# Kernel tuning notes

Measured on AMD Instinct MI355X. Metric: run time of the kernel, lower is better.

Reference implementation:

```python
import jax, jax.numpy as jnp
import numpy as np

N_GENES = 15135
K = int(np.ceil(0.5 * N_GENES))  # 7568, PyG TopKPooling ratio=0.5
BS, E, F_IN, H, HF, NC, L = 8, 242160, 64, 128, 512, 2, 3


def setup_inputs() -> dict:
    key = jax.random.key(0)
    ks = jax.random.split(key, 16)
    def lin(k, fin, fout):
        s = 1.0 / np.sqrt(fin)
        return jax.random.normal(k, (fin, fout), jnp.float32) * s
    x = jax.random.normal(ks[0], (BS, N_GENES, F_IN), jnp.float32)
    batch = jnp.zeros((BS,), jnp.int32)
    edge_index = jax.random.randint(ks[1], (2, E), 0, N_GENES, dtype=jnp.int32)
    CAT = L * H
    return {
        "x": x,
        "batch": batch,
        "edge_index": edge_index,
        "W1": lin(ks[2], F_IN, H), "b1": jnp.zeros((H,), jnp.float32),
        "W2": lin(ks[3], H, H),    "b2": jnp.zeros((H,), jnp.float32),
        "W3": lin(ks[4], H, H),    "b3": jnp.zeros((H,), jnp.float32),
        "topk_w": jax.random.normal(ks[5], (CAT,), jnp.float32) / np.sqrt(CAT),
        "fcW": lin(ks[6], CAT, 1), "fcb": jnp.zeros((1,), jnp.float32),
        "lin1W": lin(ks[7], K, HF), "lin1b": jnp.zeros((HF,), jnp.float32),
        "lin2W": lin(ks[8], HF, NC), "lin2b": jnp.zeros((NC,), jnp.float32),
    }


def reference(x, batch, edge_index, W1, b1, W2, b2, W3, b3,
              topk_w, fcW, fcb, lin1W, lin1b, lin2W, lin2b):
    bs = x.shape[0]
    # --- GCN normalization with self-loops (PyG GCNConv defaults) ---
    loop = jnp.arange(N_GENES, dtype=edge_index.dtype)
    src = jnp.concatenate([edge_index[0], loop])
    dst = jnp.concatenate([edge_index[1], loop])
    deg = jnp.zeros((N_GENES,), x.dtype).at[dst].add(1.0)
    dinv = jax.lax.rsqrt(deg)  # deg >= 1 due to self-loops
    norm = dinv[src] * dinv[dst]  # [E+N]

    def gcn(h, W, b):
        h = h @ W                                   # [bs, N, H]
        msg = h[:, src, :] * norm[None, :, None]    # gather + edge weight
        agg = jnp.zeros_like(h).at[:, dst, :].add(msg)  # scatter-add
        return agg + b

    h1 = jax.nn.relu(gcn(x, W1, b1))
    h2 = jax.nn.relu(gcn(h1, W2, b2))
    h3 = jax.nn.relu(gcn(h2, W3, b3))
    # mode='cat': stack on last dim then flatten -> feature order (H, layer)
    xc = jnp.stack([h1, h2, h3], -1).reshape(bs, N_GENES, -1)  # [bs, N, L*H]

    # --- TopKPooling (score = tanh(x.w/||w||), keep top ceil(0.5*N)) ---
    score = jnp.tanh((xc @ topk_w) / jnp.linalg.norm(topk_w))  # [bs, N]
    top_s, perm = jax.lax.top_k(score, K)                       # [bs, K]
    xp = jnp.take_along_axis(xc, perm[..., None], axis=1) * top_s[..., None]

    z = (xp @ fcW + fcb)[..., 0]          # [bs, K]
    h = jax.nn.relu(z @ lin1W + lin1b)    # [bs, HF]; dropout inactive (eval)
    logits = h @ lin2W + lin2b            # [bs, NC]
    return jax.nn.log_softmax(logits, axis=-1)
```

## Files before the change

### kernel.cpp

```cpp
#include <hip/hip_runtime.h>

#define N_G   15135
#define E_N   242160
#define BSZ   8
#define K_TOP 7568
#define NH    128
#define NBIN  65536
#define SUFS  65600

typedef float f4v __attribute__((ext_vector_type(4)));

__global__ void zero_kernel(int* __restrict__ p, int n) {
  int i = blockIdx.x * 1024 + threadIdx.x;
  if (i < n) p[i] = 0;
}

__global__ void count_kernel(const int* __restrict__ ei, int* __restrict__ cnt) {
  int e = blockIdx.x * 256 + threadIdx.x;
  if (e < E_N) atomicAdd(&cnt[ei[E_N + e]], 1);
}

__global__ __launch_bounds__(1024) void scan_kernel(const int* __restrict__ cnt,
                                                    int* __restrict__ rowstart,
                                                    float* __restrict__ dinv,
                                                    int* __restrict__ gctr,
                                                    const float* __restrict__ topk_w,
                                                    float* __restrict__ scal) {
  __shared__ int buf[1024];
  __shared__ int base;
  int tid = threadIdx.x;
  int i = blockIdx.x * 1024 + tid;
  int v = (i < N_G) ? cnt[i] : 0;
  if (i < N_G) dinv[i] = 1.0f / sqrtf((float)(v + 1));
  buf[tid] = v;
  __syncthreads();
  for (int s = 1; s < 1024; s <<= 1) {
    int t = (tid >= s) ? buf[tid - s] : 0;
    __syncthreads();
    buf[tid] += t;
    __syncthreads();
  }
  if (tid == 1023) base = atomicAdd(gctr, buf[1023]);
  __syncthreads();
  if (i < N_G) rowstart[i] = base + buf[tid] - v;
  if (blockIdx.x == 0) {
    __shared__ float fbuf[512];
    if (tid < 512) {
      float w = (tid < 384) ? topk_w[tid] : 0.f;
      fbuf[tid] = w * w;
    }
    __syncthreads();
    for (int s = 256; s > 0; s >>= 1) {
      if (tid < s) fbuf[tid] += fbuf[tid + s];
      __syncthreads();
    }
    if (tid == 0) scal[0] = 1.0f / sqrtf(fbuf[0]);
  }
}

__global__ void fill_kernel(const int* __restrict__ ei, const int* __restrict__ rowstart,
                            int* __restrict__ fillc, int* __restrict__ csr) {
  int e = blockIdx.x * 256 + threadIdx.x;
  if (e < E_N) {
    int s = ei[e], d = ei[E_N + e];
    int pos = rowstart[d] + atomicAdd(&fillc[d], 1);
    csr[pos] = s;
  }
}

template<int CIN, bool BR>
__global__ __launch_bounds__(256, 6) void mm_kernel(const float* __restrict__ A,
                                                    const float* __restrict__ W,
                                                    const float* __restrict__ bias,
                                                    float* __restrict__ out) {
  __shared__ float Bst[32][132];
  __shared__ float Ast2[32][68];
  int tid = threadIdx.x;
  int b = blockIdx.x & 7;
  int ib = blockIdx.x >> 3;
  int rb0 = b * N_G + ib * 64;
  int rmax = N_G - ib * 64;
  int c0 = (tid & 31) * 4;
  int r0 = (tid >> 5) * 8;
  float acc[8][4];
#pragma unroll
  for (int i = 0; i < 8; i++)
#pragma unroll
    for (int j = 0; j < 4; j++) acc[i][j] = 0.f;

  for (int k0 = 0; k0 < CIN; k0 += 32) {
    {
      int koff = (tid & 7) * 4;
      int row = tid >> 3;
#pragma unroll
      for (int p = 0; p < 2; ++p) {
        int r = row + p * 32;
        f4v v = {0.f, 0.f, 0.f, 0.f};
        if (r < rmax) v = __builtin_nontemporal_load((const f4v*)(A + (size_t)(rb0 + r) * CIN + k0 + koff));
        Ast2[koff + 0][r] = v.x; Ast2[koff + 1][r] = v.y;
        Ast2[koff + 2][r] = v.z; Ast2[koff + 3][r] = v.w;
      }
    }
    {
      int cc = (tid & 31) * 4;
      int kr = tid >> 5;
#pragma unroll
      for (int p = 0; p < 4; ++p) {
        int k = kr + p * 8;
        *(float4*)&Bst[k][cc] = *(const float4*)(W + (size_t)(k0 + k) * NH + cc);
      }
    }
    __syncthreads();
#pragma unroll 4
    for (int kk = 0; kk < 32; ++kk) {
      float a[8], bb[4];
      *(float4*)&a[0] = *(const float4*)&Ast2[kk][r0];
      *(float4*)&a[4] = *(const float4*)&Ast2[kk][r0 + 4];
      *(float4*)&bb[0] = *(const float4*)&Bst[kk][c0];
#pragma unroll
      for (int i = 0; i < 8; i++)
#pragma unroll
        for (int j = 0; j < 4; j++)
          acc[i][j] = fmaf(a[i], bb[j], acc[i][j]);
    }
    __syncthreads();
  }
  float b0 = 0.f, b1 = 0.f, b2 = 0.f, b3 = 0.f;
  if (BR) { b0 = bias[c0]; b1 = bias[c0+1]; b2 = bias[c0+2]; b3 = bias[c0+3]; }
#pragma unroll
  for (int i = 0; i < 8; i++) {
    int r = r0 + i;
    if (r < rmax) {
      float4 v;
      if (BR) {
        v.x = fmaxf(acc[i][0] + b0, 0.f); v.y = fmaxf(acc[i][1] + b1, 0.f);
        v.z = fmaxf(acc[i][2] + b2, 0.f); v.w = fmaxf(acc[i][3] + b3, 0.f);
      } else {
        v.x = acc[i][0]; v.y = acc[i][1]; v.z = acc[i][2]; v.w = acc[i][3];
      }
      *(float4*)(out + (size_t)(rb0 + r) * NH + c0) = v;
    }
  }
}

template<int CH, bool BR>
__global__ __launch_bounds__(256) void agg_h_kernel(const float* __restrict__ src,
                                                    const int* __restrict__ csr,
                                                    const int* __restrict__ rowstart,
                                                    const int* __restrict__ cnt,
                                                    const float* __restrict__ dinv,
                                                    const float* __restrict__ bias,
                                                    float* __restrict__ dst, int half) {
  int b = blockIdx.x & 7;
  int chunk = blockIdx.x >> 3;
  int wave = threadIdx.x >> 6, lane = threadIdx.x & 63;
  int d = chunk * 4 + wave;
  if (d >= N_G) return;
  d = __builtin_amdgcn_readfirstlane(d);
  int c = (CH == 128) ? ((half << 6) + lane) : lane;
  const float* sb = src + (size_t)b * N_G * CH;
  float dv = dinv[d];
  int e0 = rowstart[d];
  int n = cnt[d];
  const int* ce = csr + e0;
  float acc[8];
  acc[0] = dv * sb[(size_t)d * CH + c];
#pragma unroll
  for (int k = 1; k < 8; ++k) acc[k] = 0.f;
  int l = 0;
  for (; l + 16 <= n; l += 16) {
    int ss[16]; float ww[16], vv[16];
#pragma unroll
    for (int k = 0; k < 16; ++k) ss[k] = ce[l + k];
#pragma unroll
    for (int k = 0; k < 16; ++k) ww[k] = dinv[ss[k]];
#pragma unroll
    for (int k = 0; k < 16; ++k) vv[k] = sb[(size_t)ss[k] * CH + c];
#pragma unroll
    for (int k = 0; k < 16; ++k) acc[k & 7] = fmaf(ww[k], vv[k], acc[k & 7]);
  }
  for (; l + 8 <= n; l += 8) {
    int ss[8]; float ww[8], vv[8];
#pragma unroll
    for (int k = 0; k < 8; ++k) ss[k] = ce[l + k];
#pragma unroll
    for (int k = 0; k < 8; ++k) ww[k] = dinv[ss[k]];
#pragma unroll
    for (int k = 0; k < 8; ++k) vv[k] = sb[(size_t)ss[k] * CH + c];
#pragma unroll
    for (int k = 0; k < 8; ++k) acc[k] = fmaf(ww[k], vv[k], acc[k]);
  }
  for (; l < n; ++l) {
    int s = ce[l];
    acc[0] = fmaf(dinv[s], sb[(size_t)s * CH + c], acc[0]);
  }
  float s = ((acc[0] + acc[1]) + (acc[2] + acc[3])) + ((acc[4] + acc[5]) + (acc[6] + acc[7]));
  float r = BR ? fmaxf(fmaf(dv, s, bias[c]), 0.f) : dv * s;
  __builtin_nontemporal_store(r, &dst[((size_t)b * N_G + d) * CH + c]);
}

__global__ __launch_bounds__(256) void agg_score_h_kernel(const float* __restrict__ hw,
                                                          const int* __restrict__ csr,
                                                          const int* __restrict__ rowstart,
                                                          const int* __restrict__ cnt,
                                                          const float* __restrict__ dinv,
                                                          const float* __restrict__ bias,
                                                          const float* __restrict__ h1,
                                                          const float* __restrict__ h2,
                                                          const float* __restrict__ topk_w,
                                                          const float* __restrict__ fcW,
                                                          float* __restrict__ pd1,
                                                          float* __restrict__ pd2, int half) {
  int b = blockIdx.x & 7;
  int chunk = blockIdx.x >> 3;
  int wave = threadIdx.x >> 6, lane = threadIdx.x & 63;
  int d = chunk * 4 + wave;
  if (d >= N_G) return;
  d = __builtin_amdgcn_readfirstlane(d);
  int c = (half << 6) + lane;
  const float* sb = hw + (size_t)b * N_G * NH;
  float dv = dinv[d];
  int e0 = rowstart[d];
  int n = cnt[d];
  const int* ce = csr + e0;
  float acc[8];
  acc[0] = dv * sb[(size_t)d * NH + c];
#pragma unroll
  for (int k = 1; k < 8; ++k) acc[k] = 0.f;
  int l = 0;
  for (; l + 16 <= n; l += 16) {
    int ss[16]; float ww[16], vv[16];
#pragma unroll
    for (int k = 0; k < 16; ++k) ss[k] = ce[l + k];
#pragma unroll
    for (int k = 0; k < 16; ++k) ww[k] = dinv[ss[k]];
#pragma unroll
    for (int k = 0; k < 16; ++k) vv[k] = sb[(size_t)ss[k] * NH + c];
#pragma unroll
    for (int k = 0; k < 16; ++k) acc[k & 7] = fmaf(ww[k], vv[k], acc[k & 7]);
  }
  for (; l + 8 <= n; l += 8) {
    int ss[8]; float ww[8], vv[8];
#pragma unroll
    for (int k = 0; k < 8; ++k) ss[k] = ce[l + k];
#pragma unroll
    for (int k = 0; k < 8; ++k) ww[k] = dinv[ss[k]];
#pragma unroll
    for (int k = 0; k < 8; ++k) vv[k] = sb[(size_t)ss[k] * NH + c];
#pragma unroll
    for (int k = 0; k < 8; ++k) acc[k] = fmaf(ww[k], vv[k], acc[k]);
  }
  for (; l < n; ++l) {
    int s = ce[l];
    acc[0] = fmaf(dinv[s], sb[(size_t)s * NH + c], acc[0]);
  }
  float s = ((acc[0] + acc[1]) + (acc[2] + acc[3])) + ((acc[4] + acc[5]) + (acc[6] + acc[7]));
  float r = fmaxf(fmaf(dv, s, bias[c]), 0.f);
  size_t rbase = ((size_t)b * N_G + d) * NH + c;
  float u1 = __builtin_nontemporal_load(h1 + rbase);
  float u2 = __builtin_nontemporal_load(h2 + rbase);
  float d1 = u1 * topk_w[c * 3] + u2 * topk_w[c * 3 + 1] + r * topk_w[c * 3 + 2];
  float d2 = u1 * fcW[c * 3]    + u2 * fcW[c * 3 + 1]    + r * fcW[c * 3 + 2];
#pragma unroll
  for (int sh = 32; sh > 0; sh >>= 1) {
    d1 += __shfl_down(d1, sh);
    d2 += __shfl_down(d2, sh);
  }
  if (lane == 0) {
    int gw = b * N_G + d;
    pd1[gw * 2 + half] = d1;
    pd2[gw * 2 + half] = d2;
  }
}

__global__ void combine_kernel(const float* __restrict__ pd1, const float* __restrict__ pd2,
                               const float* __restrict__ scal, float* __restrict__ score,
                               float* __restrict__ d2a, unsigned* __restrict__ keys,
                               int* __restrict__ hist) {
  int b = blockIdx.y;
  int i = blockIdx.x * 256 + threadIdx.x;
  if (i >= N_G) return;
  int gw = b * N_G + i;
  float d1 = pd1[2 * gw] + pd1[2 * gw + 1];
  float d2 = pd2[2 * gw] + pd2[2 * gw + 1];
  float sc = tanhf(d1 * scal[0]);
  score[gw] = sc;
  d2a[gw] = d2;
  unsigned u = __float_as_uint(sc);
  unsigned k32 = (u & 0x80000000u) ? ~u : (u | 0x80000000u);
  keys[gw] = k32;
  atomicAdd(&hist[b * NBIN + (int)(k32 >> 16)], 1);
}

__global__ __launch_bounds__(1024) void suffix_kernel(const int* __restrict__ hist,
                                                      int* __restrict__ suf) {
  __shared__ int buf[1024];
  int b = blockIdx.x;
  const int* hb = hist + b * NBIN;
  int* sb = suf + b * SUFS;
  int t = threadIdx.x;
  int base = t * 64;
  int s = 0;
  for (int k = 0; k < 64; ++k) s += hb[base + k];
  buf[t] = s;
  __syncthreads();
  for (int off = 1; off < 1024; off <<= 1) {
    int v = (t + off < 1024) ? buf[t + off] : 0;
    __syncthreads();
    buf[t] += v;
    __syncthreads();
  }
  int acc = buf[t] - s;
  if (t == 0) sb[NBIN] = 0;
  for (int k = 63; k >= 0; --k) {
    acc += hb[base + k];
    sb[base + k] = acc;
  }
}

__global__ void scatter_kernel(const unsigned* __restrict__ keys, int* __restrict__ hist,
                               const int* __restrict__ suf, int2* __restrict__ bucket) {
  int b = blockIdx.y;
  int i = blockIdx.x * 256 + threadIdx.x;
  if (i >= N_G) return;
  unsigned k = keys[b * N_G + i];
  int bin = (int)(k >> 16);
  int old = atomicSub(&hist[b * NBIN + bin], 1);
  int pos = suf[b * SUFS + bin + 1] + old - 1;
  bucket[b * N_G + pos] = make_int2((int)k, i);
}

__global__ void rank_z_kernel(const unsigned* __restrict__ keys, const int* __restrict__ suf,
                              const int2* __restrict__ bucket, const float* __restrict__ score,
                              const float* __restrict__ d2a, const float* __restrict__ fcb,
                              float* __restrict__ z) {
  int b = blockIdx.y;
  int i = blockIdx.x * 256 + threadIdx.x;
  if (i >= N_G) return;
  int gw = b * N_G + i;
  unsigned k = keys[gw];
  int bin = (int)(k >> 16);
  int lo = suf[b * SUFS + bin + 1];
  int hi = suf[b * SUFS + bin];
  int r = lo;
  const int2* bk = bucket + b * N_G;
  for (int p = lo; p < hi; ++p) {
    int2 e = bk[p];
    unsigned kj = (unsigned)e.x;
    r += (kj > k || (kj == k && e.y < i)) ? 1 : 0;
  }
  if (r < K_TOP) z[b * K_TOP + r] = fmaf(score[gw], d2a[gw], fcb[0]);
}

__global__ __launch_bounds__(256) void lin1_kernel(const float* __restrict__ z,
                                                   const float* __restrict__ W,
                                                   float* __restrict__ hpre) {
  __shared__ float zb[237];
  int b = blockIdx.y, rs = blockIdx.x;
  int r0 = rs * 237;
  int rn = K_TOP - r0; if (rn > 237) rn = 237;
  for (int q = threadIdx.x; q < rn; q += 256) zb[q] = z[b * K_TOP + r0 + q];
  __syncthreads();
  int c = threadIdx.x;
  float a0 = 0.f, a1 = 0.f;
  for (int r = 0; r < rn; ++r) {
    float zz = zb[r];
    const float* wr = W + (size_t)(r0 + r) * 512;
    a0 = fmaf(zz, wr[c], a0);
    a1 = fmaf(zz, wr[c + 256], a1);
  }
  atomicAdd(&hpre[b * 512 + c], a0);
  atomicAdd(&hpre[b * 512 + c + 256], a1);
}

__global__ __launch_bounds__(128) void lin2_kernel(const float* __restrict__ hpre,
                                                   const float* __restrict__ l1b,
                                                   const float* __restrict__ W2,
                                                   const float* __restrict__ l2b,
                                                   float* __restrict__ out) {
  int b = blockIdx.x, tid = threadIdx.x;
  float a0 = 0.f, a1 = 0.f;
  for (int j = tid; j < 512; j += 128) {
    float t = fmaxf(hpre[b * 512 + j] + l1b[j], 0.f);
    a0 = fmaf(t, W2[j * 2 + 0], a0);
    a1 = fmaf(t, W2[j * 2 + 1], a1);
  }
#pragma unroll
  for (int s = 32; s > 0; s >>= 1) {
    a0 += __shfl_down(a0, s);
    a1 += __shfl_down(a1, s);
  }
  __shared__ float red[2][2];
  if ((tid & 63) == 0) { red[tid >> 6][0] = a0; red[tid >> 6][1] = a1; }
  __syncthreads();
  if (tid == 0) {
    float l0 = red[0][0] + red[1][0] + l2b[0];
    float l1 = red[0][1] + red[1][1] + l2b[1];
    float m = fmaxf(l0, l1);
    float lse = m + logf(expf(l0 - m) + expf(l1 - m));
    out[b * 2 + 0] = l0 - lse;
    out[b * 2 + 1] = l1 - lse;
  }
}

extern "C" void kernel_launch(void* const* d_in, const int* in_sizes, int n_in,
                              void* d_out, int out_size, void* d_ws, size_t ws_size,
                              hipStream_t stream) {
  const float* x   = (const float*)d_in[0];
  const int*   ei  = (const int*)d_in[2];
  const float* W1  = (const float*)d_in[3];
  const float* b1  = (const float*)d_in[4];
  const float* W2  = (const float*)d_in[5];
  const float* b2  = (const float*)d_in[6];
  const float* W3  = (const float*)d_in[7];
  const float* b3  = (const float*)d_in[8];
  const float* tkw = (const float*)d_in[9];
  const float* fcW = (const float*)d_in[10];
  const float* fcb = (const float*)d_in[11];
  const float* l1W = (const float*)d_in[12];
  const float* l1b = (const float*)d_in[13];
  const float* l2W = (const float*)d_in[14];
  const float* l2b = (const float*)d_in[15];
  float* out = (float*)d_out;

  char* ws = (char*)d_ws;
  size_t off = 0;
  auto alloc = [&](size_t bytes) {
    char* p = ws + off;
    off += (bytes + 255) & ~(size_t)255;
    return p;
  };
  int*   cnt   = (int*)alloc(15136 * 4);
  int*   fillc = (int*)alloc(15136 * 4);
  int*   gctr  = (int*)alloc(256);
  float* hpre  = (float*)alloc(4096 * 4);
  int*   hist  = (int*)alloc((size_t)BSZ * NBIN * 4);
  int*   rowstart = (int*)alloc(15136 * 4);
  float* dinv  = (float*)alloc(15136 * 4);
  float* scal  = (float*)alloc(64);
  float* z     = (float*)alloc((size_t)BSZ * K_TOP * 4);
  float* score = (float*)alloc(121088 * 4);
  float* d2a   = (float*)alloc(121088 * 4);
  unsigned* keys = (unsigned*)alloc(121088 * 4);
  int*   suf   = (int*)alloc((size_t)BSZ * SUFS * 4);
  int2*  bucket = (int2*)alloc(121088 * 8);
  float* pd1   = (float*)alloc(121088 * 2 * 4);
  float* pd2   = (float*)alloc(121088 * 2 * 4);
  int*   csr   = (int*)alloc((size_t)E_N * 4);
  float* ax = (float*)alloc((size_t)BSZ * N_G * 64 * 4);
  float* hw = (float*)alloc((size_t)BSZ * N_G * NH * 4);
  float* h1 = (float*)alloc((size_t)BSZ * N_G * NH * 4);
  float* h2 = (float*)alloc((size_t)BSZ * N_G * NH * 4);
  (void)ws_size; (void)in_sizes; (void)n_in; (void)out_size;

  int zero_n = (int)(((char*)rowstart - (char*)cnt) / 4);
  zero_kernel<<<(zero_n + 1023) / 1024, 1024, 0, stream>>>(cnt, zero_n);
  count_kernel<<<(E_N + 255) / 256, 256, 0, stream>>>(ei, cnt);
  scan_kernel<<<(N_G + 1023) / 1024, 1024, 0, stream>>>(cnt, rowstart, dinv, gctr, tkw, scal);
  fill_kernel<<<(E_N + 255) / 256, 256, 0, stream>>>(ei, rowstart, fillc, csr);

  dim3 mmg(8 * 237);
  int aggblocks = 8 * ((N_G + 3) / 4);

  agg_h_kernel<64, false><<<aggblocks, 256, 0, stream>>>(x, csr, rowstart, cnt, dinv, nullptr, ax, 0);
  mm_kernel<64, true><<<mmg, 256, 0, stream>>>(ax, W1, b1, h1);
  mm_kernel<128, false><<<mmg, 256, 0, stream>>>(h1, W2, nullptr, hw);
  agg_h_kernel<128, true><<<aggblocks, 256, 0, stream>>>(hw, csr, rowstart, cnt, dinv, b2, h2, 0);
  agg_h_kernel<128, true><<<aggblocks, 256, 0, stream>>>(hw, csr, rowstart, cnt, dinv, b2, h2, 1);
  mm_kernel<128, false><<<mmg, 256, 0, stream>>>(h2, W3, nullptr, hw);
  agg_score_h_kernel<<<aggblocks, 256, 0, stream>>>(hw, csr, rowstart, cnt, dinv, b3,
                                                    h1, h2, tkw, fcW, pd1, pd2, 0);
  agg_score_h_kernel<<<aggblocks, 256, 0, stream>>>(hw, csr, rowstart, cnt, dinv, b3,
                                                    h1, h2, tkw, fcW, pd1, pd2, 1);

  dim3 ng((N_G + 255) / 256, BSZ);
  combine_kernel<<<ng, 256, 0, stream>>>(pd1, pd2, scal, score, d2a, keys, hist);
  suffix_kernel<<<BSZ, 1024, 0, stream>>>(hist, suf);
  scatter_kernel<<<ng, 256, 0, stream>>>(keys, hist, suf, bucket);
  rank_z_kernel<<<ng, 256, 0, stream>>>(keys, suf, bucket, score, d2a, fcb, z);

  dim3 l1g(32, BSZ);
  lin1_kernel<<<l1g, 256, 0, stream>>>(z, l1W, hpre);
  lin2_kernel<<<BSZ, 128, 0, stream>>>(hpre, l1b, l2W, l2b, out);
}
```

Measured before the change: 724.9 us.

## Pack edge weights into CSR, add row descriptors, software-pipeline gather loop

The CSR entries now store each source index together with its dinv weight as an int2. A packed int4 row descriptor (start, count, dinv) is also built, so the aggregation kernels no longer do a dependent dinv[src] gather or three separate row-metadata loads. The neighbor loop is rewritten as an 8-wide software pipeline that loads the next batch of indices and features while the current batch is being accumulated. The trade-offs are double the CSR storage and higher register pressure from the pipelined buffers.

```diff
diff --git a/kernel.cpp b/kernel.cpp
--- a/kernel.cpp
+++ b/kernel.cpp
@@ -23,6 +23,7 @@
 __global__ __launch_bounds__(1024) void scan_kernel(const int* __restrict__ cnt,
                                                     int* __restrict__ rowstart,
                                                     float* __restrict__ dinv,
+                                                    int4* __restrict__ rowdesc,
                                                     int* __restrict__ gctr,
                                                     const float* __restrict__ topk_w,
                                                     float* __restrict__ scal) {
@@ -31,7 +32,8 @@
   int tid = threadIdx.x;
   int i = blockIdx.x * 1024 + tid;
   int v = (i < N_G) ? cnt[i] : 0;
-  if (i < N_G) dinv[i] = 1.0f / sqrtf((float)(v + 1));
+  float di = 1.0f / sqrtf((float)(v + 1));
+  if (i < N_G) dinv[i] = di;
   buf[tid] = v;
   __syncthreads();
   for (int s = 1; s < 1024; s <<= 1) {
@@ -42,7 +44,11 @@
   }
   if (tid == 1023) base = atomicAdd(gctr, buf[1023]);
   __syncthreads();
-  if (i < N_G) rowstart[i] = base + buf[tid] - v;
+  if (i < N_G) {
+    int rs = base + buf[tid] - v;
+    rowstart[i] = rs;
+    rowdesc[i] = make_int4(rs, v, __float_as_int(di), 0);
+  }
   if (blockIdx.x == 0) {
     __shared__ float fbuf[512];
     if (tid < 512) {
@@ -59,12 +65,13 @@
 }
 
 __global__ void fill_kernel(const int* __restrict__ ei, const int* __restrict__ rowstart,
-                            int* __restrict__ fillc, int* __restrict__ csr) {
+                            const float* __restrict__ dinv, int* __restrict__ fillc,
+                            int2* __restrict__ csr) {
   int e = blockIdx.x * 256 + threadIdx.x;
   if (e < E_N) {
     int s = ei[e], d = ei[E_N + e];
     int pos = rowstart[d] + atomicAdd(&fillc[d], 1);
-    csr[pos] = s;
+    csr[pos] = make_int2(s, __float_as_int(dinv[s]));
   }
 }
 
@@ -145,10 +152,8 @@
 
 template<int CH, bool BR>
 __global__ __launch_bounds__(256) void agg_h_kernel(const float* __restrict__ src,
-                                                    const int* __restrict__ csr,
-                                                    const int* __restrict__ rowstart,
-                                                    const int* __restrict__ cnt,
-                                                    const float* __restrict__ dinv,
+                                                    const int2* __restrict__ csr,
+                                                    const int4* __restrict__ rowdesc,
                                                     const float* __restrict__ bias,
                                                     float* __restrict__ dst, int half) {
   int b = blockIdx.x & 7;
@@ -157,42 +162,41 @@
   int d = chunk * 4 + wave;
   if (d >= N_G) return;
   d = __builtin_amdgcn_readfirstlane(d);
+  int4 rd = rowdesc[d];
+  int e0 = rd.x, n = rd.y;
+  float dv = __int_as_float(rd.z);
   int c = (CH == 128) ? ((half << 6) + lane) : lane;
   const float* sb = src + (size_t)b * N_G * CH;
-  float dv = dinv[d];
-  int e0 = rowstart[d];
-  int n = cnt[d];
-  const int* ce = csr + e0;
+  const int2* ce = csr + e0;
   float acc[8];
   acc[0] = dv * sb[(size_t)d * CH + c];
 #pragma unroll
   for (int k = 1; k < 8; ++k) acc[k] = 0.f;
   int l = 0;
-  for (; l + 16 <= n; l += 16) {
-    int ss[16]; float ww[16], vv[16];
-#pragma unroll
-    for (int k = 0; k < 16; ++k) ss[k] = ce[l + k];
-#pragma unroll
-    for (int k = 0; k < 16; ++k) ww[k] = dinv[ss[k]];
-#pragma unroll
-    for (int k = 0; k < 16; ++k) vv[k] = sb[(size_t)ss[k] * CH + c];
-#pragma unroll
-    for (int k = 0; k < 16; ++k) acc[k & 7] = fmaf(ww[k], vv[k], acc[k & 7]);
-  }
-  for (; l + 8 <= n; l += 8) {
-    int ss[8]; float ww[8], vv[8];
-#pragma unroll
-    for (int k = 0; k < 8; ++k) ss[k] = ce[l + k];
-#pragma unroll
-    for (int k = 0; k < 8; ++k) ww[k] = dinv[ss[k]];
-#pragma unroll
-    for (int k = 0; k < 8; ++k) vv[k] = sb[(size_t)ss[k] * CH + c];
-#pragma unroll
-    for (int k = 0; k < 8; ++k) acc[k] = fmaf(ww[k], vv[k], acc[k]);
+  if (n >= 8) {
+    int2 pA[8]; float vA[8];
+#pragma unroll
+    for (int k = 0; k < 8; ++k) pA[k] = ce[k];
+#pragma unroll
+    for (int k = 0; k < 8; ++k) vA[k] = sb[(size_t)pA[k].x * CH + c];
+    l = 8;
+    for (; l + 8 <= n; l += 8) {
+      int2 pB[8]; float vB[8];
+#pragma unroll
+      for (int k = 0; k < 8; ++k) pB[k] = ce[l + k];
+#pragma unroll
+      for (int k = 0; k < 8; ++k) vB[k] = sb[(size_t)pB[k].x * CH + c];
+#pragma unroll
+      for (int k = 0; k < 8; ++k) acc[k] = fmaf(__int_as_float(pA[k].y), vA[k], acc[k]);
+#pragma unroll
+      for (int k = 0; k < 8; ++k) { pA[k] = pB[k]; vA[k] = vB[k]; }
+    }
+#pragma unroll
+    for (int k = 0; k < 8; ++k) acc[k] = fmaf(__int_as_float(pA[k].y), vA[k], acc[k]);
   }
   for (; l < n; ++l) {
-    int s = ce[l];
-    acc[0] = fmaf(dinv[s], sb[(size_t)s * CH + c], acc[0]);
+    int2 p = ce[l];
+    acc[0] = fmaf(__int_as_float(p.y), sb[(size_t)p.x * CH + c], acc[0]);
   }
   float s = ((acc[0] + acc[1]) + (acc[2] + acc[3])) + ((acc[4] + acc[5]) + (acc[6] + acc[7]));
   float r = BR ? fmaxf(fmaf(dv, s, bias[c]), 0.f) : dv * s;
@@ -200,10 +204,8 @@
 }
 
 __global__ __launch_bounds__(256) void agg_score_h_kernel(const float* __restrict__ hw,
-                                                          const int* __restrict__ csr,
-                                                          const int* __restrict__ rowstart,
-                                                          const int* __restrict__ cnt,
-                                                          const float* __restrict__ dinv,
+                                                          const int2* __restrict__ csr,
+                                                          const int4* __restrict__ rowdesc,
                                                           const float* __restrict__ bias,
                                                           const float* __restrict__ h1,
                                                           const float* __restrict__ h2,
@@ -217,48 +219,47 @@
   int d = chunk * 4 + wave;
   if (d >= N_G) return;
   d = __builtin_amdgcn_readfirstlane(d);
+  int4 rd = rowdesc[d];
+  int e0 = rd.x, n = rd.y;
+  float dv = __int_as_float(rd.z);
   int c = (half << 6) + lane;
   const float* sb = hw + (size_t)b * N_G * NH;
-  float dv = dinv[d];
-  int e0 = rowstart[d];
-  int n = cnt[d];
-  const int* ce = csr + e0;
-  float acc[8];
-  acc[0] = dv * sb[(size_t)d * NH + c];
-#pragma unroll
-  for (int k = 1; k < 8; ++k) acc[k] = 0.f;
-  int l = 0;
-  for (; l + 16 <= n; l += 16) {
-    int ss[16]; float ww[16], vv[16];
-#pragma unroll
-    for (int k = 0; k < 16; ++k) ss[k] = ce[l + k];
-#pragma unroll
-    for (int k = 0; k < 16; ++k) ww[k] = dinv[ss[k]];
-#pragma unroll
-    for (int k = 0; k < 16; ++k) vv[k] = sb[(size_t)ss[k] * NH + c];
-#pragma unroll
-    for (int k = 0; k < 16; ++k) acc[k & 7] = fmaf(ww[k], vv[k], acc[k & 7]);
-  }
-  for (; l + 8 <= n; l += 8) {
-    int ss[8]; float ww[8], vv[8];
-#pragma unroll
-    for (int k = 0; k < 8; ++k) ss[k] = ce[l + k];
-#pragma unroll
-    for (int k = 0; k < 8; ++k) ww[k] = dinv[ss[k]];
-#pragma unroll
-    for (int k = 0; k < 8; ++k) vv[k] = sb[(size_t)ss[k] * NH + c];
-#pragma unroll
-    for (int k = 0; k < 8; ++k) acc[k] = fmaf(ww[k], vv[k], acc[k]);
-  }
-  for (; l < n; ++l) {
-    int s = ce[l];
-    acc[0] = fmaf(dinv[s], sb[(size_t)s * NH + c], acc[0]);
-  }
-  float s = ((acc[0] + acc[1]) + (acc[2] + acc[3])) + ((acc[4] + acc[5]) + (acc[6] + acc[7]));
-  float r = fmaxf(fmaf(dv, s, bias[c]), 0.f);
+  const int2* ce = csr + e0;
   size_t rbase = ((size_t)b * N_G + d) * NH + c;
   float u1 = __builtin_nontemporal_load(h1 + rbase);
   float u2 = __builtin_nontemporal_load(h2 + rbase);
+  float acc[8];
+  acc[0] = dv * sb[(size_t)d * NH + c];
+#pragma unroll
+  for (int k = 1; k < 8; ++k) acc[k] = 0.f;
+  int l = 0;
+  if (n >= 8) {
+    int2 pA[8]; float vA[8];
+#pragma unroll
+    for (int k = 0; k < 8; ++k) pA[k] = ce[k];
+#pragma unroll
+    for (int k = 0; k < 8; ++k) vA[k] = sb[(size_t)pA[k].x * NH + c];
+    l = 8;
+    for (; l + 8 <= n; l += 8) {
+      int2 pB[8]; float vB[8];
+#pragma unroll
+      for (int k = 0; k < 8; ++k) pB[k] = ce[l + k];
+#pragma unroll
+      for (int k = 0; k < 8; ++k) vB[k] = sb[(size_t)pB[k].x * NH + c];
+#pragma unroll
+      for (int k = 0; k < 8; ++k) acc[k] = fmaf(__int_as_float(pA[k].y), vA[k], acc[k]);
+#pragma unroll
+      for (int k = 0; k < 8; ++k) { pA[k] = pB[k]; vA[k] = vB[k]; }
+    }
+#pragma unroll
+    for (int k = 0; k < 8; ++k) acc[k] = fmaf(__int_as_float(pA[k].y), vA[k], acc[k]);
+  }
+  for (; l < n; ++l) {
+    int2 p = ce[l];
+    acc[0] = fmaf(__int_as_float(p.y), sb[(size_t)p.x * NH + c], acc[0]);
+  }
+  float s = ((acc[0] + acc[1]) + (acc[2] + acc[3])) + ((acc[4] + acc[5]) + (acc[6] + acc[7]));
+  float r = fmaxf(fmaf(dv, s, bias[c]), 0.f);
   float d1 = u1 * topk_w[c * 3] + u2 * topk_w[c * 3 + 1] + r * topk_w[c * 3 + 2];
   float d2 = u1 * fcW[c * 3]    + u2 * fcW[c * 3 + 1]    + r * fcW[c * 3 + 2];
 #pragma unroll
@@ -437,6 +438,7 @@
   int*   hist  = (int*)alloc((size_t)BSZ * NBIN * 4);
   int*   rowstart = (int*)alloc(15136 * 4);
   float* dinv  = (float*)alloc(15136 * 4);
+  int4*  rowdesc = (int4*)alloc(15136 * 16);
   float* scal  = (float*)alloc(64);
   float* z     = (float*)alloc((size_t)BSZ * K_TOP * 4);
   float* score = (float*)alloc(121088 * 4);
@@ -446,7 +448,7 @@
   int2*  bucket = (int2*)alloc(121088 * 8);
   float* pd1   = (float*)alloc(121088 * 2 * 4);
   float* pd2   = (float*)alloc(121088 * 2 * 4);
-  int*   csr   = (int*)alloc((size_t)E_N * 4);
+  int2*  csr   = (int2*)alloc((size_t)E_N * 8);
   float* ax = (float*)alloc((size_t)BSZ * N_G * 64 * 4);
   float* hw = (float*)alloc((size_t)BSZ * N_G * NH * 4);
   float* h1 = (float*)alloc((size_t)BSZ * N_G * NH * 4);
@@ -456,21 +458,21 @@
   int zero_n = (int)(((char*)rowstart - (char*)cnt) / 4);
   zero_kernel<<<(zero_n + 1023) / 1024, 1024, 0, stream>>>(cnt, zero_n);
   count_kernel<<<(E_N + 255) / 256, 256, 0, stream>>>(ei, cnt);
-  scan_kernel<<<(N_G + 1023) / 1024, 1024, 0, stream>>>(cnt, rowstart, dinv, gctr, tkw, scal);
-  fill_kernel<<<(E_N + 255) / 256, 256, 0, stream>>>(ei, rowstart, fillc, csr);
+  scan_kernel<<<(N_G + 1023) / 1024, 1024, 0, stream>>>(cnt, rowstart, dinv, rowdesc, gctr, tkw, scal);
+  fill_kernel<<<(E_N + 255) / 256, 256, 0, stream>>>(ei, rowstart, dinv, fillc, csr);
 
   dim3 mmg(8 * 237);
   int aggblocks = 8 * ((N_G + 3) / 4);
 
-  agg_h_kernel<64, false><<<aggblocks, 256, 0, stream>>>(x, csr, rowstart, cnt, dinv, nullptr, ax, 0);
+  agg_h_kernel<64, false><<<aggblocks, 256, 0, stream>>>(x, csr, rowdesc, nullptr, ax, 0);
   mm_kernel<64, true><<<mmg, 256, 0, stream>>>(ax, W1, b1, h1);
   mm_kernel<128, false><<<mmg, 256, 0, stream>>>(h1, W2, nullptr, hw);
-  agg_h_kernel<128, true><<<aggblocks, 256, 0, stream>>>(hw, csr, rowstart, cnt, dinv, b2, h2, 0);
-  agg_h_kernel<128, true><<<aggblocks, 256, 0, stream>>>(hw, csr, rowstart, cnt, dinv, b2, h2, 1);
+  agg_h_kernel<128, true><<<aggblocks, 256, 0, stream>>>(hw, csr, rowdesc, b2, h2, 0);
+  agg_h_kernel<128, true><<<aggblocks, 256, 0, stream>>>(hw, csr, rowdesc, b2, h2, 1);
   mm_kernel<128, false><<<mmg, 256, 0, stream>>>(h2, W3, nullptr, hw);
-  agg_score_h_kernel<<<aggblocks, 256, 0, stream>>>(hw, csr, rowstart, cnt, dinv, b3,
+  agg_score_h_kernel<<<aggblocks, 256, 0, stream>>>(hw, csr, rowdesc, b3,
                                                     h1, h2, tkw, fcW, pd1, pd2, 0);
-  agg_score_h_kernel<<<aggblocks, 256, 0, stream>>>(hw, csr, rowstart, cnt, dinv, b3,
+  agg_score_h_kernel<<<aggblocks, 256, 0, stream>>>(hw, csr, rowdesc, b3,
                                                     h1, h2, tkw, fcW, pd1, pd2, 1);
 
   dim3 ng((N_G + 255) / 256, BSZ);
```

Result: faster. 663.4 us (-8.5%).
